# Kernel optimization log

Measured on AMD Instinct MI355X. Metric: run time of the kernel, lower is better.

Reference implementation:

```python
import jax, jax.numpy as jnp
import numpy as np

N = 50000          # nodes
E = 400000         # edges (before self-loops)
F_IN = 64          # node features
H = 256            # hidden_dim
HEADS = 8
HD = 32            # head dim (hidden_dim // 8)
L = 4              # num_layers
G = 64             # num graphs
NGF = 32           # graph features per graph
NC = 2             # classes
EPS = 1e-5


def _bn(x, g, b):
    # BatchNorm1d with batch statistics (training-mode math, no dropout)
    mu = jnp.mean(x, axis=0)
    var = jnp.var(x, axis=0)
    return (x - mu) * jax.lax.rsqrt(var + EPS) * g + b


def _gat(x, src, dst, W, a_src, a_dst, bias):
    # PyG GATConv math (self-loops already included in src/dst)
    h = (x @ W).reshape(N, HEADS, HD)                      # [N,8,32]
    as_n = jnp.sum(h * a_src, axis=-1)                     # [N,8]
    ad_n = jnp.sum(h * a_dst, axis=-1)                     # [N,8]
    e = jax.nn.leaky_relu(as_n[src] + ad_n[dst], 0.2)      # [E',8]
    m = jax.ops.segment_max(e, dst, num_segments=N)        # per-dest softmax
    ex = jnp.exp(e - m[dst])
    den = jax.ops.segment_sum(ex, dst, num_segments=N)
    alpha = ex / den[dst]                                  # [E',8]
    out = jax.ops.segment_sum(alpha[:, :, None] * h[src], dst, num_segments=N)
    return out.reshape(N, HEADS * HD) + bias


def setup_inputs() -> dict:
    key = jax.random.key(0)
    ks = jax.random.split(key, 20)
    s = 0.05
    inp = {
        "x": jax.random.normal(ks[0], (N, F_IN), jnp.float32),
        "edge_index": jax.random.randint(ks[1], (2, E), 0, N, jnp.int32),
        "batch": jnp.sort(jax.random.randint(ks[2], (N,), 0, G, jnp.int32)),
        "graph_features": jax.random.normal(ks[3], (G * NGF,), jnp.float32),
        # node encoder
        "W_enc": jax.random.normal(ks[4], (F_IN, H), jnp.float32) * s,
        "b_enc": jnp.zeros((H,), jnp.float32),
        "g_enc": jnp.ones((H,), jnp.float32),
        "be_enc": jnp.zeros((H,), jnp.float32),
        # GAT layers (stacked over L layers)
        "Wg": jax.random.normal(ks[5], (L, H, H), jnp.float32) * s,
        "att_src": jax.random.normal(ks[6], (L, HEADS, HD), jnp.float32) * s,
        "att_dst": jax.random.normal(ks[7], (L, HEADS, HD), jnp.float32) * s,
        "bg": jnp.zeros((L, H), jnp.float32),
        "bn_g": jnp.ones((L, H), jnp.float32),
        "bn_b": jnp.zeros((L, H), jnp.float32),
        # classifier: (3H + NGF) -> 2H -> H -> NC
        "W1": jax.random.normal(ks[8], (3 * H + NGF, 2 * H), jnp.float32) * s,
        "b1": jnp.zeros((2 * H,), jnp.float32),
        "g1": jnp.ones((2 * H,), jnp.float32),
        "be1": jnp.zeros((2 * H,), jnp.float32),
        "W2": jax.random.normal(ks[9], (2 * H, H), jnp.float32) * s,
        "b2": jnp.zeros((H,), jnp.float32),
        "g2": jnp.ones((H,), jnp.float32),
        "be2": jnp.zeros((H,), jnp.float32),
        "W3": jax.random.normal(ks[10], (H, NC), jnp.float32) * s,
        "b3": jnp.zeros((NC,), jnp.float32),
    }
    return inp


def reference(x, edge_index, batch, graph_features, W_enc, b_enc, g_enc, be_enc,
              Wg, att_src, att_dst, bg, bn_g, bn_b,
              W1, b1, g1, be1, W2, b2, g2, be2, W3, b3):
    gf = graph_features.reshape(G, NGF)
    # add self loops (PyG GATConv default)
    loop = jnp.arange(N, dtype=edge_index.dtype)
    src = jnp.concatenate([edge_index[0], loop])
    dst = jnp.concatenate([edge_index[1], loop])

    h = jax.nn.relu(_bn(x @ W_enc + b_enc, g_enc, be_enc))  # node encoder
    for i in range(L):
        h_in = h
        h = _gat(h, src, dst, Wg[i], att_src[i], att_dst[i], bg[i])
        h = jax.nn.relu(_bn(h, bn_g[i], bn_b[i]))
        if i > 0 and i % 2 == 0:
            h = h + h_in

    # concat pooling: mean / max / sum over graphs
    cnt = jax.ops.segment_sum(jnp.ones((N,), h.dtype), batch, num_segments=G)
    s = jax.ops.segment_sum(h, batch, num_segments=G)
    mean = s / cnt[:, None]
    mx = jax.ops.segment_max(h, batch, num_segments=G)
    pooled = jnp.concatenate([mean, mx, s], axis=1)         # [G, 3H]

    z = jnp.concatenate([pooled, gf], axis=1)               # [G, 3H+NGF]
    z = jax.nn.relu(_bn(z @ W1 + b1, g1, be1))
    z = jax.nn.relu(_bn(z @ W2 + b2, g2, be2))
    return z @ W3 + b3                                      # [G, NC]
```

## Files before the change

### kernel.cpp

```cpp
#include <hip/hip_runtime.h>

#define NN 50000
#define MPAD 50048
#define EE 400000
#define EP 450000
#define FIN 64
#define HH 256
#define GG 64
#define NGFD 32
#define SB 782
#define RB 64

typedef __attribute__((ext_vector_type(8))) _Float16 f16x8;
typedef __attribute__((ext_vector_type(4))) float f32x4;

__device__ __forceinline__ unsigned short f2h(float f) {
  _Float16 h = (_Float16)f;
  return __builtin_bit_cast(unsigned short, h);
}
__device__ __forceinline__ float h2f(unsigned short s) {
  _Float16 h = __builtin_bit_cast(_Float16, s);
  return (float)h;
}

__global__ void k_init_deg(int* deg) {
  int i = blockIdx.x * 256 + threadIdx.x;
  if (i < NN) deg[i] = 1;
}
__global__ void k_hist(const int* __restrict__ dst, int* __restrict__ deg) {
  int e = blockIdx.x * 256 + threadIdx.x;
  if (e < EE) atomicAdd(&deg[dst[e]], 1);
}
__global__ void k_scan1(const int* __restrict__ deg, int* __restrict__ offs, int* __restrict__ aux) {
  __shared__ int sd[256];
  int b = blockIdx.x, t = threadIdx.x;
  int base = b * 1024 + t * 4;
  int v0 = 0, v1 = 0, v2 = 0, v3 = 0;
  if (base + 0 < NN) v0 = deg[base + 0];
  if (base + 1 < NN) v1 = deg[base + 1];
  if (base + 2 < NN) v2 = deg[base + 2];
  if (base + 3 < NN) v3 = deg[base + 3];
  sd[t] = v0 + v1 + v2 + v3;
  __syncthreads();
  for (int off = 1; off < 256; off <<= 1) {
    int x = (t >= off) ? sd[t - off] : 0;
    __syncthreads();
    sd[t] += x;
    __syncthreads();
  }
  if (t == 255) aux[b] = sd[255];
  int run = (t == 0) ? 0 : sd[t - 1];
  if (base + 0 < NN) offs[base + 0] = run; run += v0;
  if (base + 1 < NN) offs[base + 1] = run; run += v1;
  if (base + 2 < NN) offs[base + 2] = run; run += v2;
  if (base + 3 < NN) offs[base + 3] = run;
}
__global__ void k_scan2(int* aux, int nb) {
  if (threadIdx.x == 0 && blockIdx.x == 0) {
    int s = 0;
    for (int i = 0; i < nb; ++i) { int t = aux[i]; aux[i] = s; s += t; }
    aux[nb] = s;
  }
}
__global__ void k_scan3(int* __restrict__ offs, const int* __restrict__ aux) {
  int b = blockIdx.x, t = threadIdx.x;
  int base = b * 1024 + t * 4;
  int add = aux[b];
  #pragma unroll
  for (int i = 0; i < 4; ++i)
    if (base + i < NN) offs[base + i] += add;
  if (b == 0 && t == 0) offs[NN] = aux[gridDim.x];
}
__global__ void k_scatter(const int* __restrict__ srcA, const int* __restrict__ dstA,
                          int* __restrict__ cur, int* __restrict__ ssrc) {
  int e = blockIdx.x * 256 + threadIdx.x;
  if (e < EE) { int p = atomicAdd(&cur[dstA[e]], 1); ssrc[p] = srcA[e]; }
}
__global__ void k_scatter_self(int* __restrict__ cur, int* __restrict__ ssrc) {
  int i = blockIdx.x * 256 + threadIdx.x;
  if (i < NN) { int p = atomicAdd(&cur[i], 1); ssrc[p] = i; }
}

__global__ void k_bounds(const int* __restrict__ batch, int* __restrict__ start) {
  int g = threadIdx.x;
  if (g > GG) return;
  int lo = 0, hi = NN;
  while (lo < hi) { int mid = (lo + hi) >> 1; if (batch[mid] < g) lo = mid + 1; else hi = mid; }
  start[g] = lo;
}

__global__ void k_prepW(const float* __restrict__ W, unsigned short* __restrict__ WT, int K, int N) {
  __shared__ float tile[32][33];
  int l = blockIdx.z;
  const float* Wp = W + (size_t)l * K * N;
  unsigned short* Tp = WT + (size_t)l * K * N;
  int n0 = blockIdx.x * 32, k0 = blockIdx.y * 32;
  int tx = threadIdx.x & 31, ty = threadIdx.x >> 5;
  #pragma unroll
  for (int rr = 0; rr < 32; rr += 8) {
    int k = k0 + ty + rr, n = n0 + tx;
    if (k < K && n < N) tile[ty + rr][tx] = Wp[(size_t)k * N + n];
  }
  __syncthreads();
  #pragma unroll
  for (int rr = 0; rr < 32; rr += 8) {
    int n = n0 + ty + rr, k = k0 + tx;
    if (n < N && k < K) Tp[(size_t)n * K + k] = f2h(tile[tx][ty + rr]);
  }
}

__global__ void k_cvt_x(const float* __restrict__ x, unsigned short* __restrict__ xb) {
  size_t i = ((size_t)blockIdx.x * 256 + threadIdx.x) * 4;
  if (i >= (size_t)NN * FIN) return;
  float4 v = *reinterpret_cast<const float4*>(x + i);
  ushort4 o;
  o.x = f2h(v.x); o.y = f2h(v.y); o.z = f2h(v.z); o.w = f2h(v.w);
  *reinterpret_cast<ushort4*>(xb + i) = o;
}

__global__ __launch_bounds__(256) void k_mfma(const unsigned short* __restrict__ A,
                                              const unsigned short* __restrict__ BT,
                                              unsigned short* __restrict__ Cb, int K) {
  __shared__ unsigned short As[128 * 64];
  __shared__ unsigned short Bs[128 * 64];
  const int t = threadIdx.x;
  const int w = t >> 6, l = t & 63;
  const int row0 = blockIdx.x * 128;
  const int col0 = blockIdx.y * 128;
  const int wm = w & 1, wn = w >> 1;

  f32x4 acc[4][4];
  #pragma unroll
  for (int i = 0; i < 4; ++i)
    #pragma unroll
    for (int j = 0; j < 4; ++j) acc[i][j] = (f32x4){0.f, 0.f, 0.f, 0.f};

  const int lrow = w * 8 + (l >> 3);
  const int ksrc_sh = ((l & 7) ^ (lrow & 7)) << 3;

  for (int k0 = 0; k0 < K; k0 += 64) {
    #pragma unroll
    for (int rd = 0; rd < 4; ++rd) {
      int r = rd * 32 + lrow;
      const unsigned short* ga = A + (size_t)(row0 + r) * K + k0 + ksrc_sh;
      __builtin_amdgcn_global_load_lds(
          (const __attribute__((address_space(1))) void*)ga,
          (__attribute__((address_space(3))) void*)(As + (size_t)(rd * 32 + w * 8) * 64),
          16, 0, 0);
    }
    #pragma unroll
    for (int rd = 0; rd < 4; ++rd) {
      int r = rd * 32 + lrow;
      const unsigned short* gb = BT + (size_t)(col0 + r) * K + k0 + ksrc_sh;
      __builtin_amdgcn_global_load_lds(
          (const __attribute__((address_space(1))) void*)gb,
          (__attribute__((address_space(3))) void*)(Bs + (size_t)(rd * 32 + w * 8) * 64),
          16, 0, 0);
    }
    __syncthreads();

    const char* AsB = (const char*)As;
    const char* BsB = (const char*)Bs;
    #pragma unroll
    for (int ks = 0; ks < 2; ++ks) {
      f16x8 af[4], bfr[4];
      #pragma unroll
      for (int i = 0; i < 4; ++i) {
        int ar = wm * 64 + i * 16 + (l & 15);
        int ab = ar * 128 + ((ks * 64 + (l >> 4) * 16) ^ ((ar & 7) << 4));
        af[i] = *(const f16x8*)(AsB + ab);
        int br = wn * 64 + i * 16 + (l & 15);
        int bb = br * 128 + ((ks * 64 + (l >> 4) * 16) ^ ((br & 7) << 4));
        bfr[i] = *(const f16x8*)(BsB + bb);
      }
      #pragma unroll
      for (int i = 0; i < 4; ++i)
        #pragma unroll
        for (int j = 0; j < 4; ++j)
          acc[i][j] = __builtin_amdgcn_mfma_f32_16x16x32_f16(af[i], bfr[j], acc[i][j], 0, 0, 0);
    }
    __syncthreads();
  }

  #pragma unroll
  for (int i = 0; i < 4; ++i) {
    int rbase = row0 + wm * 64 + i * 16 + ((l >> 4) * 4);
    #pragma unroll
    for (int j = 0; j < 4; ++j) {
      int c = col0 + wn * 64 + j * 16 + (l & 15);
      #pragma unroll
      for (int r = 0; r < 4; ++r) {
        int rr = rbase + r;
        if (rr < NN) Cb[(size_t)rr * HH + c] = f2h(acc[i][j][r]);
      }
    }
  }
}

__global__ void k_attdot(const unsigned short* __restrict__ hp, const float* __restrict__ a_s,
                         const float* __restrict__ a_d, float* __restrict__ asn,
                         float* __restrict__ adn) {
  int lane = threadIdx.x & 63;
  int n = blockIdx.x * 4 + (threadIdx.x >> 6);
  if (n >= NN) return;
  ushort4 v = *reinterpret_cast<const ushort4*>(hp + (size_t)n * HH + lane * 4);
  float4 s4 = *reinterpret_cast<const float4*>(a_s + lane * 4);
  float4 d4 = *reinterpret_cast<const float4*>(a_d + lane * 4);
  float x0 = h2f(v.x), x1 = h2f(v.y), x2 = h2f(v.z), x3 = h2f(v.w);
  float ps = x0 * s4.x + x1 * s4.y + x2 * s4.z + x3 * s4.w;
  float pd = x0 * d4.x + x1 * d4.y + x2 * d4.z + x3 * d4.w;
  ps += __shfl_xor(ps, 1); ps += __shfl_xor(ps, 2); ps += __shfl_xor(ps, 4);
  pd += __shfl_xor(pd, 1); pd += __shfl_xor(pd, 2); pd += __shfl_xor(pd, 4);
  if ((lane & 7) == 0) {
    asn[n * 8 + (lane >> 3)] = ps;
    adn[n * 8 + (lane >> 3)] = pd;
  }
}

__global__ __launch_bounds__(256) void k_gat_agg(const int* __restrict__ offs, const int* __restrict__ ssrc,
                                                 const float* __restrict__ asn, const float* __restrict__ adn,
                                                 const unsigned short* __restrict__ hp,
                                                 float* __restrict__ outp) {
  int lane = threadIdx.x & 63;
  int n = blockIdx.x * 4 + (threadIdx.x >> 6);
  if (n >= NN) return;
  int hd = lane >> 3;
  float adh = adn[n * 8 + hd];
  int e0 = offs[n], e1 = offs[n + 1];
  float m = -1e30f, den = 0.f;
  float4 acc = make_float4(0.f, 0.f, 0.f, 0.f);

  auto step = [&](float av, ushort4 hv) {
    float e = fmaxf(av, 0.2f * av);
    float mn = fmaxf(m, e);
    float sc = __expf(m - mn);
    float p  = __expf(e - mn);
    den = den * sc + p;
    acc.x = acc.x * sc + p * h2f(hv.x);
    acc.y = acc.y * sc + p * h2f(hv.y);
    acc.z = acc.z * sc + p * h2f(hv.z);
    acc.w = acc.w * sc + p * h2f(hv.w);
    m = mn;
  };

  int k = e0;
  for (; k + 4 <= e1; k += 4) {
    int s0 = ssrc[k], s1 = ssrc[k + 1], s2 = ssrc[k + 2], s3 = ssrc[k + 3];
    ushort4 h0 = *reinterpret_cast<const ushort4*>(hp + (size_t)s0 * HH + lane * 4);
    ushort4 h1 = *reinterpret_cast<const ushort4*>(hp + (size_t)s1 * HH + lane * 4);
    ushort4 h2 = *reinterpret_cast<const ushort4*>(hp + (size_t)s2 * HH + lane * 4);
    ushort4 h3 = *reinterpret_cast<const ushort4*>(hp + (size_t)s3 * HH + lane * 4);
    float a0 = asn[s0 * 8 + hd] + adh;
    float a1 = asn[s1 * 8 + hd] + adh;
    float a2 = asn[s2 * 8 + hd] + adh;
    float a3 = asn[s3 * 8 + hd] + adh;
    step(a0, h0); step(a1, h1); step(a2, h2); step(a3, h3);
  }
  for (; k < e1; ++k) {
    int s = ssrc[k];
    ushort4 hv = *reinterpret_cast<const ushort4*>(hp + (size_t)s * HH + lane * 4);
    float av = asn[s * 8 + hd] + adh;
    step(av, hv);
  }
  float rden = 1.f / den;
  float4 o = make_float4(acc.x * rden, acc.y * rden, acc.z * rden, acc.w * rden);
  *reinterpret_cast<float4*>(outp + (size_t)n * HH + lane * 4) = o;
}

__global__ void k_cstat_f32(const float* __restrict__ x, float* __restrict__ pst) {
  int c = threadIdx.x, b = blockIdx.x;
  int r0 = b * 64, r1 = min(r0 + 64, NN);
  float s = 0.f, q = 0.f;
  for (int r = r0; r < r1; ++r) {
    float v = x[(size_t)r * HH + c];
    s += v; q += v * v;
  }
  pst[b * 512 + c] = s;
  pst[b * 512 + 256 + c] = q;
}
__global__ void k_cstat_h(const unsigned short* __restrict__ x, float* __restrict__ pst) {
  int c = threadIdx.x, b = blockIdx.x;
  int r0 = b * 64, r1 = min(r0 + 64, NN);
  float s = 0.f, q = 0.f;
  for (int r = r0; r < r1; ++r) {
    float v = h2f(x[(size_t)r * HH + c]);
    s += v; q += v * v;
  }
  pst[b * 512 + c] = s;
  pst[b * 512 + 256 + c] = q;
}
__global__ void k_redstat1(const float* __restrict__ pst, float* __restrict__ pst2) {
  int t = threadIdx.x, p = blockIdx.x;
  int b0 = p * 13, b1 = min(b0 + 13, SB);
  float s0 = 0.f, s1 = 0.f;
  for (int b = b0; b < b1; ++b) {
    s0 += pst[b * 512 + t];
    s1 += pst[b * 512 + 256 + t];
  }
  pst2[p * 512 + t] = s0;
  pst2[p * 512 + 256 + t] = s1;
}
__global__ void k_redstat2(const float* __restrict__ pst2, float* __restrict__ stats) {
  int c = blockIdx.x * 256 + threadIdx.x;
  float s = 0.f;
  #pragma unroll
  for (int b = 0; b < RB; ++b) s += pst2[b * 512 + c];
  stats[c] = s;
}

__global__ void k_bnap_h(const unsigned short* __restrict__ x, const float* __restrict__ stats,
                         const float* __restrict__ g, const float* __restrict__ b,
                         unsigned short* __restrict__ ybf) {
  size_t i = ((size_t)blockIdx.x * 256 + threadIdx.x) * 4;
  if (i >= (size_t)NN * HH) return;
  ushort4 v = *reinterpret_cast<const ushort4*>(x + i);
  int c = (int)(i & 255);
  const float invN = 1.f / (float)NN;
  float vv[4] = {h2f(v.x), h2f(v.y), h2f(v.z), h2f(v.w)};
  ushort4 bo;
  float o[4];
  #pragma unroll
  for (int j = 0; j < 4; ++j) {
    int cc = c + j;
    float mean = stats[cc] * invN;
    float var = stats[HH + cc] * invN - mean * mean;
    float rs = rsqrtf(var + 1e-5f);
    float val = (vv[j] - mean) * rs * g[cc] + b[cc];
    o[j] = fmaxf(val, 0.f);
  }
  bo.x = f2h(o[0]); bo.y = f2h(o[1]); bo.z = f2h(o[2]); bo.w = f2h(o[3]);
  *reinterpret_cast<ushort4*>(ybf + i) = bo;
}
__global__ void k_bnap_f(const float* __restrict__ x, const float* __restrict__ stats,
                         const float* __restrict__ g, const float* __restrict__ b,
                         const unsigned short* res, unsigned short* __restrict__ ybf) {
  size_t i = ((size_t)blockIdx.x * 256 + threadIdx.x) * 4;
  if (i >= (size_t)NN * HH) return;
  float4 v = *reinterpret_cast<const float4*>(x + i);
  int c = (int)(i & 255);
  const float invN = 1.f / (float)NN;
  float vv[4] = {v.x, v.y, v.z, v.w};
  float rv[4] = {0.f, 0.f, 0.f, 0.f};
  if (res) {
    ushort4 r4 = *reinterpret_cast<const ushort4*>(res + i);
    rv[0] = h2f(r4.x); rv[1] = h2f(r4.y); rv[2] = h2f(r4.z); rv[3] = h2f(r4.w);
  }
  float o[4];
  #pragma unroll
  for (int j = 0; j < 4; ++j) {
    int cc = c + j;
    float mean = stats[cc] * invN;
    float var = stats[HH + cc] * invN - mean * mean;
    float rs = rsqrtf(var + 1e-5f);
    float val = (vv[j] - mean) * rs * g[cc] + b[cc];
    val = fmaxf(val, 0.f) + rv[j];
    o[j] = val;
  }
  ushort4 bo;
  bo.x = f2h(o[0]); bo.y = f2h(o[1]); bo.z = f2h(o[2]); bo.w = f2h(o[3]);
  *reinterpret_cast<ushort4*>(ybf + i) = bo;
}

__global__ void k_pool(const unsigned short* __restrict__ h, const int* __restrict__ batch,
                       float* __restrict__ gsum, float* __restrict__ gmax) {
  int c = threadIdx.x;
  int r0 = blockIdx.x * 64, r1 = min(r0 + 64, NN);
  if (r0 >= r1) return;
  int curg = batch[r0];
  float s = 0.f, mx = 0.f;
  for (int r = r0; r < r1; ++r) {
    int g = batch[r];
    if (g != curg) {
      atomicAdd(&gsum[curg * HH + c], s);
      atomicMax((int*)&gmax[curg * HH + c], __float_as_int(mx));
      s = 0.f; mx = 0.f; curg = g;
    }
    float v = h2f(h[(size_t)r * HH + c]);
    s += v; mx = fmaxf(mx, v);
  }
  atomicAdd(&gsum[curg * HH + c], s);
  atomicMax((int*)&gmax[curg * HH + c], __float_as_int(mx));
}
__global__ void k_buildz(const float* __restrict__ gsum, const float* __restrict__ gmax,
                         const int* __restrict__ start, const float* __restrict__ gf,
                         float* __restrict__ z) {
  int g = blockIdx.x;
  float invc = 1.f / (float)(start[g + 1] - start[g]);
  for (int c = threadIdx.x; c < 800; c += 256) {
    float v;
    if (c < 256)      v = gsum[g * HH + c] * invc;
    else if (c < 512) v = gmax[g * HH + (c - 256)];
    else if (c < 768) v = gsum[g * HH + (c - 512)];
    else              v = gf[g * NGFD + (c - 768)];
    z[g * 800 + c] = v;
  }
}

__global__ __launch_bounds__(256) void k_linsplit(const float* __restrict__ zin,
                                                  const float* __restrict__ W,
                                                  float* __restrict__ pacc, int K, int OC) {
  __shared__ float zs[64][65];
  int t = threadIdx.x;
  int kc = blockIdx.y, k0 = kc * 64;
  int kmax = min(64, K - k0);
  for (int idx = t; idx < 64 * 64; idx += 256) {
    int r = idx >> 6, k = idx & 63;
    zs[r][k] = (k < kmax) ? zin[(size_t)r * K + k0 + k] : 0.f;
  }
  __syncthreads();
  int jl = t & 15, rq = t >> 4;
  int j = blockIdx.x * 16 + jl;
  float acc[4] = {0.f, 0.f, 0.f, 0.f};
  int k = 0;
  for (; k + 8 <= kmax; k += 8) {
    float wv[8];
    #pragma unroll
    for (int u = 0; u < 8; ++u) wv[u] = W[(size_t)(k0 + k + u) * OC + j];
    #pragma unroll
    for (int u = 0; u < 8; ++u)
      #pragma unroll
      for (int rr = 0; rr < 4; ++rr) acc[rr] += zs[rq * 4 + rr][k + u] * wv[u];
  }
  for (; k < kmax; ++k) {
    float wv = W[(size_t)(k0 + k) * OC + j];
    #pragma unroll
    for (int rr = 0; rr < 4; ++rr) acc[rr] += zs[rq * 4 + rr][k] * wv;
  }
  float* pp = pacc + ((size_t)kc * OC + j) * 64 + rq * 4;
  #pragma unroll
  for (int rr = 0; rr < 4; ++rr) pp[rr] = acc[rr];
}

__global__ __launch_bounds__(64) void k_linred(const float* __restrict__ pacc,
                                               const float* __restrict__ g,
                                               const float* __restrict__ be,
                                               float* __restrict__ zout, int OC, int KC) {
  int j = blockIdx.x, r = threadIdx.x;
  float s = 0.f;
  for (int kc = 0; kc < KC; ++kc) s += pacc[((size_t)kc * OC + j) * 64 + r];
  float S = s, Q = s * s;
  #pragma unroll
  for (int off = 32; off >= 1; off >>= 1) {
    S += __shfl_xor(S, off);
    Q += __shfl_xor(Q, off);
  }
  float mu = S * (1.f / 64.f);
  float var = Q * (1.f / 64.f) - mu * mu;
  float scv = rsqrtf(var + 1e-5f) * g[j];
  float sh = be[j] - mu * scv;
  zout[(size_t)r * OC + j] = fmaxf(s * scv + sh, 0.f);
}

__global__ void k_final(const float* __restrict__ z2, const float* __restrict__ W3,
                        const float* __restrict__ b3, float* __restrict__ out) {
  int t = threadIdx.x;
  if (t >= 128) return;
  int i = t >> 1, j = t & 1;
  float acc = b3[j];
  for (int k = 0; k < 256; ++k) acc += z2[i * 256 + k] * W3[k * 2 + j];
  out[i * 2 + j] = acc;
}

extern "C" void kernel_launch(void* const* d_in, const int* in_sizes, int n_in,
                              void* d_out, int out_size, void* d_ws, size_t ws_size,
                              hipStream_t stream) {
  const float* x      = (const float*)d_in[0];
  const int*   ei     = (const int*)d_in[1];
  const int*   batch  = (const int*)d_in[2];
  const float* gf     = (const float*)d_in[3];
  const float* W_enc  = (const float*)d_in[4];
  const float* g_enc  = (const float*)d_in[6];
  const float* be_enc = (const float*)d_in[7];
  const float* Wg     = (const float*)d_in[8];
  const float* att_s  = (const float*)d_in[9];
  const float* att_d  = (const float*)d_in[10];
  const float* bn_g   = (const float*)d_in[12];
  const float* bn_b   = (const float*)d_in[13];
  const float* W1     = (const float*)d_in[14];
  const float* g1     = (const float*)d_in[16];
  const float* be1    = (const float*)d_in[17];
  const float* W2     = (const float*)d_in[18];
  const float* g2     = (const float*)d_in[20];
  const float* be2    = (const float*)d_in[21];
  const float* W3     = (const float*)d_in[22];
  const float* b3     = (const float*)d_in[23];
  float* out = (float*)d_out;

  char* w = (char*)d_ws;
  auto alloc = [&](size_t bytes) { char* p = w; w += (bytes + 255) & ~(size_t)255; return p; };
  float*          Cc   = (float*)alloc((size_t)MPAD * HH * 4);
  unsigned short* A_bf = (unsigned short*)alloc((size_t)MPAD * HH * 2);
  unsigned short* hp   = (unsigned short*)alloc((size_t)MPAD * HH * 2);
  unsigned short* x_bf = (unsigned short*)alloc((size_t)MPAD * FIN * 2);
  float* asn  = (float*)alloc((size_t)NN * 8 * 4);
  float* adn  = (float*)alloc((size_t)NN * 8 * 4);
  int*   deg  = (int*)alloc((size_t)NN * 4);
  int*   offs = (int*)alloc((size_t)(NN + 1) * 4);
  int*   cur  = (int*)alloc((size_t)NN * 4);
  int*   ssrc = (int*)alloc((size_t)EP * 4);
  float* pst  = (float*)alloc((size_t)SB * 512 * 4);
  float* pst2 = (float*)alloc((size_t)RB * 512 * 4);
  float* stats= (float*)alloc(512 * 4);
  int*   aux  = (int*)alloc(64 * 4);
  int*   start= (int*)alloc(65 * 4);
  unsigned short* WencT = (unsigned short*)alloc((size_t)HH * FIN * 2);
  unsigned short* WgT   = (unsigned short*)alloc((size_t)4 * HH * HH * 2);
  float* gsum = (float*)alloc((size_t)GG * HH * 4);
  float* gmax = (float*)alloc((size_t)GG * HH * 4);
  float* zb   = (float*)alloc((size_t)GG * 800 * 4);
  float* z1   = (float*)alloc((size_t)GG * 512 * 4);
  float* z2   = (float*)alloc((size_t)GG * 256 * 4);
  float* pacc = (float*)alloc((size_t)13 * 512 * 64 * 4);

  const int* e_src = ei;
  const int* e_dst = ei + EE;

  k_init_deg<<<196, 256, 0, stream>>>(deg);
  k_hist<<<1563, 256, 0, stream>>>(e_dst, deg);
  k_scan1<<<49, 256, 0, stream>>>(deg, offs, aux);
  k_scan2<<<1, 64, 0, stream>>>(aux, 49);
  k_scan3<<<49, 256, 0, stream>>>(offs, aux);
  hipMemcpyAsync(cur, offs, (size_t)NN * 4, hipMemcpyDeviceToDevice, stream);
  k_scatter<<<1563, 256, 0, stream>>>(e_src, e_dst, cur, ssrc);
  k_scatter_self<<<196, 256, 0, stream>>>(cur, ssrc);
  k_bounds<<<1, 128, 0, stream>>>(batch, start);

  k_prepW<<<dim3(8, 2, 1), 256, 0, stream>>>(W_enc, WencT, FIN, HH);
  k_prepW<<<dim3(8, 8, 4), 256, 0, stream>>>(Wg, WgT, HH, HH);
  k_cvt_x<<<3125, 256, 0, stream>>>(x, x_bf);

  dim3 mg(MPAD / 128, 2);

  k_mfma<<<mg, 256, 0, stream>>>(x_bf, WencT, hp, FIN);
  k_cstat_h<<<SB, 256, 0, stream>>>(hp, pst);
  k_redstat1<<<RB, 256, 0, stream>>>(pst, pst2);
  k_redstat2<<<2, 256, 0, stream>>>(pst2, stats);
  k_bnap_h<<<12500, 256, 0, stream>>>(hp, stats, g_enc, be_enc, A_bf);

  for (int l = 0; l < 4; ++l) {
    k_mfma<<<mg, 256, 0, stream>>>(A_bf, WgT + (size_t)l * HH * HH, hp, HH);
    k_attdot<<<12500, 256, 0, stream>>>(hp, att_s + l * HH, att_d + l * HH, asn, adn);
    k_gat_agg<<<12500, 256, 0, stream>>>(offs, ssrc, asn, adn, hp, Cc);
    k_cstat_f32<<<SB, 256, 0, stream>>>(Cc, pst);
    k_redstat1<<<RB, 256, 0, stream>>>(pst, pst2);
    k_redstat2<<<2, 256, 0, stream>>>(pst2, stats);
    k_bnap_f<<<12500, 256, 0, stream>>>(Cc, stats, bn_g + l * HH, bn_b + l * HH,
                                        (l == 2) ? A_bf : nullptr, A_bf);
  }

  hipMemsetAsync(gsum, 0, (size_t)GG * HH * 4, stream);
  hipMemsetAsync(gmax, 0, (size_t)GG * HH * 4, stream);
  k_pool<<<SB, 256, 0, stream>>>(A_bf, batch, gsum, gmax);
  k_buildz<<<GG, 256, 0, stream>>>(gsum, gmax, start, gf, zb);
  k_linsplit<<<dim3(32, 13), 256, 0, stream>>>(zb, W1, pacc, 800, 512);
  k_linred<<<512, 64, 0, stream>>>(pacc, g1, be1, z1, 512, 13);
  k_linsplit<<<dim3(16, 8), 256, 0, stream>>>(z1, W2, pacc, 512, 256);
  k_linred<<<256, 64, 0, stream>>>(pacc, g2, be2, z2, 256, 8);
  k_final<<<1, 128, 0, stream>>>(z2, W3, b3, out);
}
```

Baseline: 643.6 us.

## Store GAT aggregation output in fp16 and drop online softmax max tracking

```diff
diff --git a/kernel.cpp b/kernel.cpp
--- a/kernel.cpp
+++ b/kernel.cpp
@@ -220,27 +220,24 @@
 __global__ __launch_bounds__(256) void k_gat_agg(const int* __restrict__ offs, const int* __restrict__ ssrc,
                                                  const float* __restrict__ asn, const float* __restrict__ adn,
                                                  const unsigned short* __restrict__ hp,
-                                                 float* __restrict__ outp) {
+                                                 unsigned short* __restrict__ outp) {
   int lane = threadIdx.x & 63;
   int n = blockIdx.x * 4 + (threadIdx.x >> 6);
   if (n >= NN) return;
   int hd = lane >> 3;
   float adh = adn[n * 8 + hd];
   int e0 = offs[n], e1 = offs[n + 1];
-  float m = -1e30f, den = 0.f;
+  float den = 0.f;
   float4 acc = make_float4(0.f, 0.f, 0.f, 0.f);
 
   auto step = [&](float av, ushort4 hv) {
     float e = fmaxf(av, 0.2f * av);
-    float mn = fmaxf(m, e);
-    float sc = __expf(m - mn);
-    float p  = __expf(e - mn);
-    den = den * sc + p;
-    acc.x = acc.x * sc + p * h2f(hv.x);
-    acc.y = acc.y * sc + p * h2f(hv.y);
-    acc.z = acc.z * sc + p * h2f(hv.z);
-    acc.w = acc.w * sc + p * h2f(hv.w);
-    m = mn;
+    float p = __expf(fminf(e, 40.f));
+    den += p;
+    acc.x += p * h2f(hv.x);
+    acc.y += p * h2f(hv.y);
+    acc.z += p * h2f(hv.z);
+    acc.w += p * h2f(hv.w);
   };
 
   int k = e0;
@@ -263,21 +260,12 @@
     step(av, hv);
   }
   float rden = 1.f / den;
-  float4 o = make_float4(acc.x * rden, acc.y * rden, acc.z * rden, acc.w * rden);
-  *reinterpret_cast<float4*>(outp + (size_t)n * HH + lane * 4) = o;
-}
-
-__global__ void k_cstat_f32(const float* __restrict__ x, float* __restrict__ pst) {
-  int c = threadIdx.x, b = blockIdx.x;
-  int r0 = b * 64, r1 = min(r0 + 64, NN);
-  float s = 0.f, q = 0.f;
-  for (int r = r0; r < r1; ++r) {
-    float v = x[(size_t)r * HH + c];
-    s += v; q += v * v;
-  }
-  pst[b * 512 + c] = s;
-  pst[b * 512 + 256 + c] = q;
-}
+  ushort4 o;
+  o.x = f2h(acc.x * rden); o.y = f2h(acc.y * rden);
+  o.z = f2h(acc.z * rden); o.w = f2h(acc.w * rden);
+  *reinterpret_cast<ushort4*>(outp + (size_t)n * HH + lane * 4) = o;
+}
+
 __global__ void k_cstat_h(const unsigned short* __restrict__ x, float* __restrict__ pst) {
   int c = threadIdx.x, b = blockIdx.x;
   int r0 = b * 64, r1 = min(r0 + 64, NN);
@@ -310,36 +298,13 @@
 
 __global__ void k_bnap_h(const unsigned short* __restrict__ x, const float* __restrict__ stats,
                          const float* __restrict__ g, const float* __restrict__ b,
-                         unsigned short* __restrict__ ybf) {
+                         const unsigned short* res, unsigned short* __restrict__ ybf) {
   size_t i = ((size_t)blockIdx.x * 256 + threadIdx.x) * 4;
   if (i >= (size_t)NN * HH) return;
   ushort4 v = *reinterpret_cast<const ushort4*>(x + i);
   int c = (int)(i & 255);
   const float invN = 1.f / (float)NN;
   float vv[4] = {h2f(v.x), h2f(v.y), h2f(v.z), h2f(v.w)};
-  ushort4 bo;
-  float o[4];
-  #pragma unroll
-  for (int j = 0; j < 4; ++j) {
-    int cc = c + j;
-    float mean = stats[cc] * invN;
-    float var = stats[HH + cc] * invN - mean * mean;
-    float rs = rsqrtf(var + 1e-5f);
-    float val = (vv[j] - mean) * rs * g[cc] + b[cc];
-    o[j] = fmaxf(val, 0.f);
-  }
-  bo.x = f2h(o[0]); bo.y = f2h(o[1]); bo.z = f2h(o[2]); bo.w = f2h(o[3]);
-  *reinterpret_cast<ushort4*>(ybf + i) = bo;
-}
-__global__ void k_bnap_f(const float* __restrict__ x, const float* __restrict__ stats,
-                         const float* __restrict__ g, const float* __restrict__ b,
-                         const unsigned short* res, unsigned short* __restrict__ ybf) {
-  size_t i = ((size_t)blockIdx.x * 256 + threadIdx.x) * 4;
-  if (i >= (size_t)NN * HH) return;
-  float4 v = *reinterpret_cast<const float4*>(x + i);
-  int c = (int)(i & 255);
-  const float invN = 1.f / (float)NN;
-  float vv[4] = {v.x, v.y, v.z, v.w};
   float rv[4] = {0.f, 0.f, 0.f, 0.f};
   if (res) {
     ushort4 r4 = *reinterpret_cast<const ushort4*>(res + i);
@@ -488,7 +453,7 @@
 
   char* w = (char*)d_ws;
   auto alloc = [&](size_t bytes) { char* p = w; w += (bytes + 255) & ~(size_t)255; return p; };
-  float*          Cc   = (float*)alloc((size_t)MPAD * HH * 4);
+  unsigned short* Cc_h = (unsigned short*)alloc((size_t)MPAD * HH * 2);
   unsigned short* A_bf = (unsigned short*)alloc((size_t)MPAD * HH * 2);
   unsigned short* hp   = (unsigned short*)alloc((size_t)MPAD * HH * 2);
   unsigned short* x_bf = (unsigned short*)alloc((size_t)MPAD * FIN * 2);
@@ -535,16 +500,16 @@
   k_cstat_h<<<SB, 256, 0, stream>>>(hp, pst);
   k_redstat1<<<RB, 256, 0, stream>>>(pst, pst2);
   k_redstat2<<<2, 256, 0, stream>>>(pst2, stats);
-  k_bnap_h<<<12500, 256, 0, stream>>>(hp, stats, g_enc, be_enc, A_bf);
+  k_bnap_h<<<12500, 256, 0, stream>>>(hp, stats, g_enc, be_enc, nullptr, A_bf);
 
   for (int l = 0; l < 4; ++l) {
     k_mfma<<<mg, 256, 0, stream>>>(A_bf, WgT + (size_t)l * HH * HH, hp, HH);
     k_attdot<<<12500, 256, 0, stream>>>(hp, att_s + l * HH, att_d + l * HH, asn, adn);
-    k_gat_agg<<<12500, 256, 0, stream>>>(offs, ssrc, asn, adn, hp, Cc);
-    k_cstat_f32<<<SB, 256, 0, stream>>>(Cc, pst);
+    k_gat_agg<<<12500, 256, 0, stream>>>(offs, ssrc, asn, adn, hp, Cc_h);
+    k_cstat_h<<<SB, 256, 0, stream>>>(Cc_h, pst);
     k_redstat1<<<RB, 256, 0, stream>>>(pst, pst2);
     k_redstat2<<<2, 256, 0, stream>>>(pst2, stats);
-    k_bnap_f<<<12500, 256, 0, stream>>>(Cc, stats, bn_g + l * HH, bn_b + l * HH,
+    k_bnap_h<<<12500, 256, 0, stream>>>(Cc_h, stats, bn_g + l * HH, bn_b + l * HH,
                                         (l == 2) ? A_bf : nullptr, A_bf);
   }
 
```

Result: faster. 618.7 us (-3.9%).
